# Optimization experiments

Measured on AMD Instinct MI355X. Metric: run time of the kernel, lower is better.

Reference implementation:

```python
import jax, jax.numpy as jnp
import numpy as np

EPS = 1e-12
RANK = 16


def setup_inputs() -> dict:
    key = jax.random.key(0)
    ks = jax.random.split(key, 7)
    bs, seq, d_in, d_out = 8, 2048, 4096, 4096
    n_tasks, n_splits, n_skills, rank = 256, 1, 8, RANK
    return {
        "x": jax.random.normal(ks[0], (bs, seq, d_in), dtype=jnp.float32),
        "task_ids": jax.random.randint(ks[1], (bs,), 0, n_tasks, dtype=jnp.int64 if jax.config.jax_enable_x64 else jnp.int32),
        "weight": jax.random.normal(ks[2], (d_out, d_in), dtype=jnp.float32) * 0.02,
        "bias": jax.random.normal(ks[3], (d_out,), dtype=jnp.float32) * 0.02,
        "module_logits": jax.random.normal(ks[4], (n_tasks, n_splits * n_skills), dtype=jnp.float32) * 0.001,
        "lora_a": jax.random.normal(ks[5], (n_splits, n_skills, d_in // n_splits, rank), dtype=jnp.float32) * 0.01,
        "lora_b": jax.random.normal(ks[6], (n_splits, n_skills, rank, d_out // n_splits), dtype=jnp.float32) * 0.01,
    }


def reference(x, task_ids, weight, bias, module_logits, lora_a, lora_b):
    bs = x.shape[0]
    n_splits, n_skills, _, rank = lora_a.shape
    d_in = n_splits * lora_a.shape[2]
    d_out = n_splits * lora_b.shape[3]
    # PolytroponSelector (eval path): sigmoid then sum-normalize over skills
    logits = module_logits[task_ids].reshape(bs, n_splits, n_skills)
    mw = jax.nn.sigmoid(logits)
    mw = mw / (mw.sum(axis=-1, keepdims=True) + EPS)  # [b, q, s]
    # Mix LoRA skill matrices per example
    A = jnp.einsum('bqs,qsdr->bqdr', mw, lora_a).reshape(bs, d_in, rank)
    B = jnp.einsum('bqs,qsrd->bqrd', mw, lora_b)
    B = jnp.transpose(B, (0, 2, 1, 3)).reshape(bs, rank, d_out)
    adapter_out = jnp.einsum('btr,brd->btd', jnp.einsum('bti,bir->btr', x, A), B) / rank
    base = jnp.einsum('bti,oi->bto', x, weight) + bias
    return base + adapter_out
```

## Files before the change

kernel.cpp:

```cpp
#include <hip/hip_runtime.h>
#include <hip/hip_bf16.h>
#include <cstdint>
#include <cstddef>

typedef __bf16 bf16_t;
typedef __bf16 bf16x8 __attribute__((ext_vector_type(8)));
typedef float f32x4 __attribute__((ext_vector_type(4)));

#define GLP(p)  (const __attribute__((address_space(1))) void*)(p)
#define LDSP(p) (__attribute__((address_space(3))) void*)(p)

static constexpr int BS   = 8;
static constexpr int SEQ  = 2048;
static constexpr int DIN  = 4096;
static constexpr int DOUT = 4096;
static constexpr int NSK  = 8;
static constexpr int RANK = 16;
static constexpr int MTOT = BS * SEQ;

static __device__ __forceinline__ bf16x8 cvt8(float4 v0, float4 v1) {
    bf16x8 o;
    o[0] = (bf16_t)v0.x; o[1] = (bf16_t)v0.y; o[2] = (bf16_t)v0.z; o[3] = (bf16_t)v0.w;
    o[4] = (bf16_t)v1.x; o[5] = (bf16_t)v1.y; o[6] = (bf16_t)v1.z; o[7] = (bf16_t)v1.w;
    return o;
}

__global__ __launch_bounds__(256) void mix_kernel(
    const float* __restrict__ logits, const int* __restrict__ task_ids,
    const float* __restrict__ lora_a, const float* __restrict__ lora_b,
    bf16_t* __restrict__ Abt, bf16_t* __restrict__ Btp) {
    int b = blockIdx.y;
    int c = blockIdx.x;
    int tid = threadIdx.x;

    int t = task_ids[b];
    float w[NSK]; float sum = 0.f;
#pragma unroll
    for (int s = 0; s < NSK; ++s) {
        float lg = logits[t * NSK + s];
        float sg = 1.f / (1.f + __expf(-lg));
        w[s] = sg; sum += sg;
    }
    float inv = 1.f / (sum + 1e-12f);
#pragma unroll
    for (int s = 0; s < NSK; ++s) w[s] *= inv;

    {
        int r = tid & 15, kk = tid >> 4;
#pragma unroll
        for (int i = 0; i < 4; ++i) {
            int k = c * 64 + i * 16 + kk;
            float acc = 0.f;
#pragma unroll
            for (int s = 0; s < NSK; ++s)
                acc += w[s] * lora_a[((size_t)s * DIN + k) * RANK + r];
            Abt[((size_t)b * RANK + r) * DIN + k] = (bf16_t)acc;
        }
    }
    {
        int n = c * 64 + (tid & 63);
        int r0 = tid >> 6;
#pragma unroll
        for (int i = 0; i < 4; ++i) {
            int rr = r0 + i * 4;
            float acc = 0.f;
#pragma unroll
            for (int s = 0; s < NSK; ++s)
                acc += w[s] * lora_b[((size_t)s * RANK + rr) * DOUT + n];
            Btp[((size_t)b * DOUT + n) * 32 + rr] = (bf16_t)acc;
            Btp[((size_t)b * DOUT + n) * 32 + 16 + rr] = (bf16_t)0.f;
        }
    }
}

__global__ __launch_bounds__(256) void convw_kernel(const float* __restrict__ W,
                                                    bf16_t* __restrict__ Wb) {
    size_t g = (size_t)blockIdx.x * 256 + threadIdx.x;
    const float4* src = (const float4*)W;
    float4 v0 = src[g * 2], v1 = src[g * 2 + 1];
    *(bf16x8*)(Wb + g * 8) = cvt8(v0, v1);
}

template<bool XPRE>
__global__ __launch_bounds__(256) void tconv_kernel(
    const float* __restrict__ x, const bf16_t* __restrict__ Abt,
    bf16_t* __restrict__ xb, bf16_t* __restrict__ tpad) {
    __shared__ __align__(16) bf16_t As[64 * 64];
    __shared__ __align__(16) bf16_t Aa[16 * 64];

    int row0 = blockIdx.x * 64;
    int b = row0 >> 11;
    int tid = threadIdx.x;
    int w = tid >> 6, l = tid & 63;
    const bf16_t* Ab = Abt + (size_t)b * RANK * DIN;

    f32x4 acc = {0.f, 0.f, 0.f, 0.f};

    for (int k0 = 0; k0 < DIN; k0 += 64) {
#pragma unroll
        for (int i = 0; i < 2; ++i) {
            int flat = i * 256 + tid;
            int row = flat >> 3, c8 = flat & 7;
            const float* src = x + (size_t)(row0 + row) * DIN + k0 + c8 * 8;
            float4 v0 = *(const float4*)src;
            float4 v1 = *(const float4*)(src + 4);
            bf16x8 o = cvt8(v0, v1);
            *(bf16x8*)(&As[flat * 8]) = o;
            if (XPRE)
                *(bf16x8*)(xb + (size_t)(row0 + row) * DIN + k0 + c8 * 8) = o;
        }
        if (tid < 128) {
            int r = tid >> 3, c8 = tid & 7;
            __builtin_amdgcn_global_load_lds(GLP(Ab + (size_t)r * DIN + k0 + c8 * 8),
                                             LDSP(&Aa[tid * 8]), 16, 0, 0);
        }
        __syncthreads();
#pragma unroll
        for (int s = 0; s < 2; ++s) {
            int kr = s * 32 + (l >> 4) * 8;
            bf16x8 a = *(const bf16x8*)(&As[(w * 16 + (l & 15)) * 64 + kr]);
            bf16x8 bb = *(const bf16x8*)(&Aa[(l & 15) * 64 + kr]);
            acc = __builtin_amdgcn_mfma_f32_16x16x32_bf16(a, bb, acc, 0, 0, 0);
        }
        __syncthreads();
    }
    int r = l & 15;
    int rowb = w * 16 + (l >> 4) * 4;
#pragma unroll
    for (int j = 0; j < 4; ++j) {
        int gm = row0 + rowb + j;
        tpad[(size_t)gm * 32 + r] = (bf16_t)(acc[j] * 0.0625f);
        tpad[(size_t)gm * 32 + 16 + r] = (bf16_t)0.f;
    }
}

struct P8 { int wm, wn, l4, l15, l; };

__device__ __forceinline__ const bf16x8* ldsAddr(const bf16_t* buf, int row, int g) {
    return (const bf16x8*)(buf + row * 64 + ((g ^ (row & 7)) << 3));
}

template<int MH, int NH, bool LA, bool LB, typename F>
__device__ __forceinline__ void phaseX(const bf16_t* bufA, const bf16_t* bufB,
                                       const P8& p, bf16x8 (&ar)[4][2],
                                       bf16x8 (&br)[2][2], f32x4 (&acc)[8][4],
                                       F&& pre) {
    if (LA) {
#pragma unroll
        for (int i = 0; i < 4; ++i) {
            int row = p.wm * 128 + MH * 64 + i * 16 + p.l15;
#pragma unroll
            for (int s = 0; s < 2; ++s)
                ar[i][s] = *ldsAddr(bufA, row, s * 4 + p.l4);
        }
    }
    if (LB) {
#pragma unroll
        for (int j = 0; j < 2; ++j) {
            int row = p.wn * 64 + NH * 32 + j * 16 + p.l15;
#pragma unroll
            for (int s = 0; s < 2; ++s)
                br[j][s] = *ldsAddr(bufB, row, s * 4 + p.l4);
        }
    }
    pre();
    __builtin_amdgcn_s_barrier();
    asm volatile("s_waitcnt lgkmcnt(0)" ::: "memory");
    __builtin_amdgcn_sched_barrier(0);
    __builtin_amdgcn_s_setprio(1);
#pragma unroll
    for (int s = 0; s < 2; ++s)
#pragma unroll
        for (int i = 0; i < 4; ++i)
#pragma unroll
            for (int j = 0; j < 2; ++j)
                acc[MH * 4 + i][NH * 2 + j] = __builtin_amdgcn_mfma_f32_16x16x32_bf16(
                    ar[i][s], br[j][s], acc[MH * 4 + i][NH * 2 + j], 0, 0, 0);
    __builtin_amdgcn_s_setprio(0);
    __builtin_amdgcn_s_barrier();
}

__global__ __launch_bounds__(512) void gemm8_kernel(
    const bf16_t* __restrict__ xb, const bf16_t* __restrict__ Wb,
    const float* __restrict__ bias,
    const bf16_t* __restrict__ tpad, const bf16_t* __restrict__ Btp,
    float* __restrict__ out) {
    __shared__ __align__(16) bf16_t lds[2][2][256 * 64];

    int tid = threadIdx.x;
    int w = tid >> 6, l = tid & 63;
    P8 p{w >> 2, w & 3, l >> 4, l & 15, l};

    int orig = blockIdx.x;
    int id = (orig & 7) * 128 + (orig >> 3);
    int mb = id >> 4, nb = id & 15;
    int row0 = mb * 256, col0 = nb * 256;
    int b = row0 >> 11;

    f32x4 acc[8][4] = {};
    bf16x8 ar[4][2], br[2][2];

    auto stageA = [&](int kt, int c) {
        int k0 = kt * 64;
#pragma unroll
        for (int g = 0; g < 4; ++g) {
            int row = w * 32 + g * 8 + (l >> 3);
            int sc = (l & 7) ^ (row & 7);
            __builtin_amdgcn_global_load_lds(
                GLP(xb + (size_t)(row0 + row) * DIN + k0 + sc * 8),
                LDSP(&lds[c][0][(w * 32 + g * 8) * 64 + l * 8]), 16, 0, 0);
        }
    };
    auto stageB = [&](int kt, int c) {
        int k0 = kt * 64;
#pragma unroll
        for (int g = 0; g < 4; ++g) {
            int row = w * 32 + g * 8 + (l >> 3);
            int sc = (l & 7) ^ (row & 7);
            __builtin_amdgcn_global_load_lds(
                GLP(Wb + (size_t)(col0 + row) * DIN + k0 + sc * 8),
                LDSP(&lds[c][1][(w * 32 + g * 8) * 64 + l * 8]), 16, 0, 0);
        }
    };
    auto stageAdp = [&]() {
#pragma unroll
        for (int g = 0; g < 2; ++g) {
            int flat = g * 512 + tid;
            int row = flat >> 2, ch = flat & 3;
            __builtin_amdgcn_global_load_lds(
                GLP(tpad + (size_t)(row0 + row) * 32 + ch * 8),
                LDSP(&lds[0][0][flat * 8]), 16, 0, 0);
        }
#pragma unroll
        for (int g = 0; g < 2; ++g) {
            int flat = g * 512 + tid;
            int row = flat >> 2, ch = flat & 3;
            __builtin_amdgcn_global_load_lds(
                GLP(Btp + ((size_t)b * DOUT + col0 + row) * 32 + ch * 8),
                LDSP(&lds[0][1][flat * 8]), 16, 0, 0);
        }
    };

    stageA(0, 0);
    stageB(0, 0);

#pragma unroll 1
    for (int j = 0; j < 64; ++j) {
        int c = j & 1;
        if (j < 63) stageA(j + 1, c ^ 1);
        else        stageAdp();
        asm volatile("s_waitcnt vmcnt(4)" ::: "memory");
        __builtin_amdgcn_sched_barrier(0);
        __builtin_amdgcn_s_barrier();

        const bf16_t* bufA = &lds[c][0][0];
        const bf16_t* bufB = &lds[c][1][0];
        phaseX<0, 0, true,  true >(bufA, bufB, p, ar, br, acc, [&] {});
        phaseX<0, 1, false, true >(bufA, bufB, p, ar, br, acc,
                                   [&] { if (j < 63) stageB(j + 1, c ^ 1); });
        phaseX<1, 1, true,  false>(bufA, bufB, p, ar, br, acc, [&] {});
        phaseX<1, 0, false, true >(bufA, bufB, p, ar, br, acc, [&] {});
    }

    asm volatile("s_waitcnt vmcnt(0)" ::: "memory");
    __builtin_amdgcn_s_barrier();
    {
        const bf16_t* A0 = &lds[0][0][0];
        const bf16_t* B0 = &lds[0][1][0];
        bf16x8 aa[8]; bf16x8 bb[4];
#pragma unroll
        for (int i = 0; i < 8; ++i)
            aa[i] = *(const bf16x8*)(A0 + (p.wm * 128 + i * 16 + p.l15) * 32 + p.l4 * 8);
#pragma unroll
        for (int j = 0; j < 4; ++j)
            bb[j] = *(const bf16x8*)(B0 + (p.wn * 64 + j * 16 + p.l15) * 32 + p.l4 * 8);
#pragma unroll
        for (int i = 0; i < 8; ++i)
#pragma unroll
            for (int j = 0; j < 4; ++j)
                acc[i][j] = __builtin_amdgcn_mfma_f32_16x16x32_bf16(aa[i], bb[j], acc[i][j], 0, 0, 0);
    }

#pragma unroll
    for (int i = 0; i < 8; ++i) {
        int gm = row0 + p.wm * 128 + i * 16 + p.l4 * 4;
#pragma unroll
        for (int j = 0; j < 4; ++j) {
            int gn = col0 + p.wn * 64 + j * 16 + p.l15;
            float bsv = bias[gn];
#pragma unroll
            for (int q = 0; q < 4; ++q)
                out[(size_t)(gm + q) * DOUT + gn] = acc[i][j][q] + bsv;
        }
    }
}

template<bool WPRE>
__global__ __launch_bounds__(256) void gemm_kernel(
    const float* __restrict__ xf,
    const float* __restrict__ Wf, const bf16_t* __restrict__ Wb,
    const float* __restrict__ bias,
    const bf16_t* __restrict__ tpad, const bf16_t* __restrict__ Btp,
    float* __restrict__ out) {
    __shared__ __align__(16) bf16_t As[128 * 64];
    __shared__ __align__(16) bf16_t Bs[128 * 64];

    int orig = blockIdx.x;
    int id = (orig & 7) * 512 + (orig >> 3);
    int mb = id >> 5, nb = id & 31;
    int row0 = mb * 128, col0 = nb * 128;
    int b = row0 >> 11;

    int tid = threadIdx.x;
    int w = tid >> 6, l = tid & 63;
    int wm = w >> 1, wn = w & 1;

    f32x4 acc[4][4] = {};

    for (int k0 = 0; k0 < DIN; k0 += 64) {
#pragma unroll
        for (int i = 0; i < 4; ++i) {
            int flat = i * 256 + tid;
            int row = flat >> 3, c8 = flat & 7;
            const float* src = xf + (size_t)(row0 + row) * DIN + k0 + c8 * 8;
            float4 v0 = *(const float4*)src;
            float4 v1 = *(const float4*)(src + 4);
            *(bf16x8*)(&As[flat * 8]) = cvt8(v0, v1);
        }
        if constexpr (WPRE) {
#pragma unroll
            for (int i = 0; i < 4; ++i) {
                int flat = i * 256 + tid;
                int row = flat >> 3, c8 = flat & 7;
                __builtin_amdgcn_global_load_lds(
                    GLP(Wb + (size_t)(col0 + row) * DIN + k0 + c8 * 8),
                    LDSP(&Bs[flat * 8]), 16, 0, 0);
            }
        } else {
#pragma unroll
            for (int i = 0; i < 4; ++i) {
                int flat = i * 256 + tid;
                int row = flat >> 3, c8 = flat & 7;
                const float* src = Wf + (size_t)(col0 + row) * DIN + k0 + c8 * 8;
                float4 v0 = *(const float4*)src;
                float4 v1 = *(const float4*)(src + 4);
                *(bf16x8*)(&Bs[flat * 8]) = cvt8(v0, v1);
            }
        }
        __syncthreads();
#pragma unroll
        for (int s = 0; s < 2; ++s) {
            int kr = s * 32 + (l >> 4) * 8;
            bf16x8 a[4], bf[4];
#pragma unroll
            for (int i = 0; i < 4; ++i)
                a[i] = *(const bf16x8*)(&As[(wm * 64 + i * 16 + (l & 15)) * 64 + kr]);
#pragma unroll
            for (int j = 0; j < 4; ++j)
                bf[j] = *(const bf16x8*)(&Bs[(wn * 64 + j * 16 + (l & 15)) * 64 + kr]);
#pragma unroll
            for (int i = 0; i < 4; ++i)
#pragma unroll
                for (int j = 0; j < 4; ++j)
                    acc[i][j] = __builtin_amdgcn_mfma_f32_16x16x32_bf16(a[i], bf[j], acc[i][j], 0, 0, 0);
        }
        __syncthreads();
    }

    {
#pragma unroll
        for (int i = 0; i < 2; ++i) {
            int flat = i * 256 + tid;
            int row = flat >> 2, c8 = flat & 3;
            __builtin_amdgcn_global_load_lds(
                GLP(tpad + (size_t)(row0 + row) * 32 + c8 * 8),
                LDSP(&As[flat * 8]), 16, 0, 0);
            __builtin_amdgcn_global_load_lds(
                GLP(Btp + ((size_t)b * DOUT + col0 + row) * 32 + c8 * 8),
                LDSP(&Bs[flat * 8]), 16, 0, 0);
        }
        __syncthreads();
        int kr = (l >> 4) * 8;
        bf16x8 a[4], bf[4];
#pragma unroll
        for (int i = 0; i < 4; ++i)
            a[i] = *(const bf16x8*)(&As[(wm * 64 + i * 16 + (l & 15)) * 32 + kr]);
#pragma unroll
        for (int j = 0; j < 4; ++j)
            bf[j] = *(const bf16x8*)(&Bs[(wn * 64 + j * 16 + (l & 15)) * 32 + kr]);
#pragma unroll
        for (int i = 0; i < 4; ++i)
#pragma unroll
            for (int j = 0; j < 4; ++j)
                acc[i][j] = __builtin_amdgcn_mfma_f32_16x16x32_bf16(a[i], bf[j], acc[i][j], 0, 0, 0);
    }

#pragma unroll
    for (int i = 0; i < 4; ++i) {
        int gm = row0 + wm * 64 + i * 16 + (l >> 4) * 4;
#pragma unroll
        for (int j = 0; j < 4; ++j) {
            int gn = col0 + wn * 64 + j * 16 + (l & 15);
            float bs = bias[gn];
#pragma unroll
            for (int q = 0; q < 4; ++q)
                out[(size_t)(gm + q) * DOUT + gn] = acc[i][j][q] + bs;
        }
    }
}

extern "C" void kernel_launch(void* const* d_in, const int* in_sizes, int n_in,
                              void* d_out, int out_size, void* d_ws, size_t ws_size,
                              hipStream_t stream) {
    const float* x        = (const float*)d_in[0];
    const int*   task_ids = (const int*)d_in[1];
    const float* W        = (const float*)d_in[2];
    const float* bias     = (const float*)d_in[3];
    const float* logits   = (const float*)d_in[4];
    const float* lora_a   = (const float*)d_in[5];
    const float* lora_b   = (const float*)d_in[6];
    float* out = (float*)d_out;

    char* ws = (char*)d_ws;
    size_t off = 0;
    auto alloc = [&](size_t bytes) {
        char* p = ws + off;
        off += (bytes + 255) & ~(size_t)255;
        return p;
    };
    bf16_t* Abt  = (bf16_t*)alloc((size_t)BS * RANK * DIN * 2);
    bf16_t* Btp  = (bf16_t*)alloc((size_t)BS * DOUT * 32 * 2);
    bf16_t* tpad = (bf16_t*)alloc((size_t)MTOT * 32 * 2);
    bf16_t* Wb   = (bf16_t*)alloc((size_t)DOUT * DIN * 2);
    size_t w_end = off;
    bf16_t* xb   = (bf16_t*)alloc((size_t)MTOT * DIN * 2);
    size_t full_end = off;

    bool wpre = ws_size >= w_end;
    bool xpre = ws_size >= full_end;

    mix_kernel<<<dim3(64, 8), 256, 0, stream>>>(logits, task_ids, lora_a, lora_b, Abt, Btp);
    if (wpre)
        convw_kernel<<<(DOUT * DIN / 8) / 256, 256, 0, stream>>>(W, Wb);
    if (xpre)
        tconv_kernel<true><<<MTOT / 64, 256, 0, stream>>>(x, Abt, xb, tpad);
    else
        tconv_kernel<false><<<MTOT / 64, 256, 0, stream>>>(x, Abt, nullptr, tpad);

    if (xpre) {
        int nblk = (MTOT / 256) * (DOUT / 256);
        gemm8_kernel<<<nblk, 512, 0, stream>>>(xb, Wb, bias, tpad, Btp, out);
    } else {
        int nblk = (MTOT / 128) * (DOUT / 128);
        if (wpre)
            gemm_kernel<true><<<nblk, 256, 0, stream>>>(x, W, Wb, bias, tpad, Btp, out);
        else
            gemm_kernel<false><<<nblk, 256, 0, stream>>>(x, W, Wb, bias, tpad, Btp, out);
    }
}
```

Measured before the change: 650.6 us.

## Replace per-phase barriers with one barrier per k-step and free scheduling

Removes the four-phase ping-pong structure, which used two workgroup barriers and setprio per phase, and keeps a single barrier at the top and one after the vmcnt wait per k iteration. LDS fragment loads are issued with separate register sets (a0/a1/b0/b1) so the compiler can overlap them with MFMAs. The launch bounds now request 2 blocks per CU. Fewer barriers should cut synchronisation stalls, but this gives up the explicit wave interleaving. The extra fragment registers plus the occupancy hint may cause register spills.

```diff
diff --git a/kernel.cpp b/kernel.cpp
--- a/kernel.cpp
+++ b/kernel.cpp
@@ -140,47 +140,7 @@
     return (const bf16x8*)(buf + row * 64 + ((g ^ (row & 7)) << 3));
 }
 
-template<int MH, int NH, bool LA, bool LB, typename F>
-__device__ __forceinline__ void phaseX(const bf16_t* bufA, const bf16_t* bufB,
-                                       const P8& p, bf16x8 (&ar)[4][2],
-                                       bf16x8 (&br)[2][2], f32x4 (&acc)[8][4],
-                                       F&& pre) {
-    if (LA) {
-#pragma unroll
-        for (int i = 0; i < 4; ++i) {
-            int row = p.wm * 128 + MH * 64 + i * 16 + p.l15;
-#pragma unroll
-            for (int s = 0; s < 2; ++s)
-                ar[i][s] = *ldsAddr(bufA, row, s * 4 + p.l4);
-        }
-    }
-    if (LB) {
-#pragma unroll
-        for (int j = 0; j < 2; ++j) {
-            int row = p.wn * 64 + NH * 32 + j * 16 + p.l15;
-#pragma unroll
-            for (int s = 0; s < 2; ++s)
-                br[j][s] = *ldsAddr(bufB, row, s * 4 + p.l4);
-        }
-    }
-    pre();
-    __builtin_amdgcn_s_barrier();
-    asm volatile("s_waitcnt lgkmcnt(0)" ::: "memory");
-    __builtin_amdgcn_sched_barrier(0);
-    __builtin_amdgcn_s_setprio(1);
-#pragma unroll
-    for (int s = 0; s < 2; ++s)
-#pragma unroll
-        for (int i = 0; i < 4; ++i)
-#pragma unroll
-            for (int j = 0; j < 2; ++j)
-                acc[MH * 4 + i][NH * 2 + j] = __builtin_amdgcn_mfma_f32_16x16x32_bf16(
-                    ar[i][s], br[j][s], acc[MH * 4 + i][NH * 2 + j], 0, 0, 0);
-    __builtin_amdgcn_s_setprio(0);
-    __builtin_amdgcn_s_barrier();
-}
-
-__global__ __launch_bounds__(512) void gemm8_kernel(
+__global__ __launch_bounds__(512, 2) void gemm8_kernel(
     const bf16_t* __restrict__ xb, const bf16_t* __restrict__ Wb,
     const float* __restrict__ bias,
     const bf16_t* __restrict__ tpad, const bf16_t* __restrict__ Btp,
@@ -198,7 +158,6 @@
     int b = row0 >> 11;
 
     f32x4 acc[8][4] = {};
-    bf16x8 ar[4][2], br[2][2];
 
     auto stageA = [&](int kt, int c) {
         int k0 = kt * 64;
@@ -241,29 +200,89 @@
         }
     };
 
+    auto loadA = [&](const bf16_t* bufA, int MH, bf16x8 (&ar)[4][2]) {
+#pragma unroll
+        for (int i = 0; i < 4; ++i) {
+            int row = p.wm * 128 + MH * 64 + i * 16 + p.l15;
+#pragma unroll
+            for (int s = 0; s < 2; ++s)
+                ar[i][s] = *ldsAddr(bufA, row, s * 4 + p.l4);
+        }
+    };
+    auto loadB = [&](const bf16_t* bufB, int NH, bf16x8 (&br)[2][2]) {
+#pragma unroll
+        for (int jj = 0; jj < 2; ++jj) {
+            int row = p.wn * 64 + NH * 32 + jj * 16 + p.l15;
+#pragma unroll
+            for (int s = 0; s < 2; ++s)
+                br[jj][s] = *ldsAddr(bufB, row, s * 4 + p.l4);
+        }
+    };
+
     stageA(0, 0);
     stageB(0, 0);
 
 #pragma unroll 1
     for (int j = 0; j < 64; ++j) {
         int c = j & 1;
+        __builtin_amdgcn_sched_barrier(0);
+        __builtin_amdgcn_s_barrier();
+        __builtin_amdgcn_sched_barrier(0);
         if (j < 63) stageA(j + 1, c ^ 1);
         else        stageAdp();
         asm volatile("s_waitcnt vmcnt(4)" ::: "memory");
         __builtin_amdgcn_sched_barrier(0);
         __builtin_amdgcn_s_barrier();
+        __builtin_amdgcn_sched_barrier(0);
 
         const bf16_t* bufA = &lds[c][0][0];
         const bf16_t* bufB = &lds[c][1][0];
-        phaseX<0, 0, true,  true >(bufA, bufB, p, ar, br, acc, [&] {});
-        phaseX<0, 1, false, true >(bufA, bufB, p, ar, br, acc,
-                                   [&] { if (j < 63) stageB(j + 1, c ^ 1); });
-        phaseX<1, 1, true,  false>(bufA, bufB, p, ar, br, acc, [&] {});
-        phaseX<1, 0, false, true >(bufA, bufB, p, ar, br, acc, [&] {});
+
+        bf16x8 a0[4][2], a1[4][2], b0[2][2], b1[2][2];
+        loadA(bufA, 0, a0);
+        loadB(bufB, 0, b0);
+        if (j < 63) stageB(j + 1, c ^ 1);
+
+#pragma unroll
+        for (int s = 0; s < 2; ++s)
+#pragma unroll
+            for (int i = 0; i < 4; ++i)
+#pragma unroll
+                for (int jj = 0; jj < 2; ++jj)
+                    acc[i][jj] = __builtin_amdgcn_mfma_f32_16x16x32_bf16(
+                        a0[i][s], b0[jj][s], acc[i][jj], 0, 0, 0);
+        loadB(bufB, 1, b1);
+#pragma unroll
+        for (int s = 0; s < 2; ++s)
+#pragma unroll
+            for (int i = 0; i < 4; ++i)
+#pragma unroll
+                for (int jj = 0; jj < 2; ++jj)
+                    acc[i][2 + jj] = __builtin_amdgcn_mfma_f32_16x16x32_bf16(
+                        a0[i][s], b1[jj][s], acc[i][2 + jj], 0, 0, 0);
+        loadA(bufA, 1, a1);
+#pragma unroll
+        for (int s = 0; s < 2; ++s)
+#pragma unroll
+            for (int i = 0; i < 4; ++i)
+#pragma unroll
+                for (int jj = 0; jj < 2; ++jj)
+                    acc[4 + i][2 + jj] = __builtin_amdgcn_mfma_f32_16x16x32_bf16(
+                        a1[i][s], b1[jj][s], acc[4 + i][2 + jj], 0, 0, 0);
+#pragma unroll
+        for (int s = 0; s < 2; ++s)
+#pragma unroll
+            for (int i = 0; i < 4; ++i)
+#pragma unroll
+                for (int jj = 0; jj < 2; ++jj)
+                    acc[4 + i][jj] = __builtin_amdgcn_mfma_f32_16x16x32_bf16(
+                        a1[i][s], b0[jj][s], acc[4 + i][jj], 0, 0, 0);
     }
 
     asm volatile("s_waitcnt vmcnt(0)" ::: "memory");
+    __builtin_amdgcn_sched_barrier(0);
     __builtin_amdgcn_s_barrier();
+    __builtin_amdgcn_sched_barrier(0);
     {
         const bf16_t* A0 = &lds[0][0][0];
         const bf16_t* B0 = &lds[0][1][0];
```

Measured after the change: 602.5 us (median of 2 runs). 1.08x faster.
